# Kernel tuning notes

Hardware: AMD Instinct MI355X
Metric: run time of the kernel (lower is better)

## Reference

```python
import jax, jax.numpy as jnp
import numpy as np

TEMPERATURE = 11.313708498984761  # sqrt(128)


def setup_inputs() -> dict:
    key = jax.random.key(0)
    kq, kk, kv = jax.random.split(key, 3)
    b, n, m, d, dv = 16, 2048, 2048, 128, 128
    return {
        "queries": jax.random.normal(kq, (b, n, d), dtype=jnp.float32),
        "keys": jax.random.normal(kk, (b, m, d), dtype=jnp.float32),
        "values": jax.random.normal(kv, (b, m, dv), dtype=jnp.float32),
    }


def reference(queries, keys, values):
    # scores: [b, n, m]
    scores = jnp.einsum('bnd,bmd->bnm', queries, keys) / TEMPERATURE
    attn = jax.nn.softmax(scores, axis=2)
    # out: [b, n, d']
    return jnp.einsum('bnm,bmd->bnd', attn, values)
```

## Files before the change

kernel.cpp:

```cpp
#include <hip/hip_runtime.h>
#include <hip/hip_bf16.h>


#define BATCH 16
#define SEQ   2048
#define DIM   128

typedef short bf16x8 __attribute__((ext_vector_type(8)));
typedef float f32x16 __attribute__((ext_vector_type(16)));

static __device__ inline unsigned pk2(float lo, float hi) {
  union { float f; unsigned u; } a, b;
  a.f = lo; b.f = hi;
  return ((b.u + 0x8000u) & 0xffff0000u) | ((a.u + 0x8000u) >> 16);
}
static __device__ inline unsigned short f2bf(float f) {
  union { float f; unsigned u; } v; v.f = f;
  return (unsigned short)((v.u + 0x8000u) >> 16);
}
static __device__ inline float fast_exp2(float x) {
#if __has_builtin(__builtin_amdgcn_exp2f)
  return __builtin_amdgcn_exp2f(x);
#else
  return exp2f(x);
#endif
}

__global__ __launch_bounds__(256)
void prep_kernel(const float* __restrict__ K, const float* __restrict__ V,
                 unsigned short* __restrict__ Kb, unsigned short* __restrict__ Vt,
                 float scale) {
  const int bx = blockIdx.x, tid = threadIdx.x;
  if (bx < 2048) {
    size_t idx = (size_t)bx * 256 + tid;
    const float4* kf = (const float4*)K;
    float4 a = kf[idx * 2], c = kf[idx * 2 + 1];
    uint4 o;
    o.x = pk2(a.x * scale, a.y * scale);
    o.y = pk2(a.z * scale, a.w * scale);
    o.z = pk2(c.x * scale, c.y * scale);
    o.w = pk2(c.z * scale, c.w * scale);
    ((uint4*)Kb)[idx] = o;
  } else {
    __shared__ float tile[128][33];
    const int vb = bx - 2048;
    const int b = vb >> 6, r = vb & 63;
    const int m0 = (r & 15) * 128, d0 = (r >> 4) * 32;
    const int c = tid & 7, mr = tid >> 3;
    const float* src = V + ((size_t)(b * SEQ) + m0) * DIM + d0;
#pragma unroll
    for (int it = 0; it < 4; ++it) {
      int m = it * 32 + mr;
      float4 x = *(const float4*)(src + (size_t)m * DIM + c * 4);
      tile[m][c * 4 + 0] = x.x; tile[m][c * 4 + 1] = x.y;
      tile[m][c * 4 + 2] = x.z; tile[m][c * 4 + 3] = x.w;
    }
    __syncthreads();
    const int dr = tid >> 3, s = tid & 7;
    unsigned short* dst = Vt + ((size_t)(b * DIM) + d0 + dr) * SEQ + m0;
#pragma unroll
    for (int it = 0; it < 2; ++it) {
      int slot = it * 8 + s;
      uint4 o;
      o.x = pk2(tile[slot * 8 + 0][dr], tile[slot * 8 + 1][dr]);
      o.y = pk2(tile[slot * 8 + 2][dr], tile[slot * 8 + 3][dr]);
      o.z = pk2(tile[slot * 8 + 4][dr], tile[slot * 8 + 5][dr]);
      o.w = pk2(tile[slot * 8 + 6][dr], tile[slot * 8 + 7][dr]);
      *(uint4*)(dst + slot * 8) = o;
    }
  }
}

#define KS_OFF 0
#define VS_OFF 8704
#define PS_OFF 17920

__global__ __launch_bounds__(256, 2)
void attn_kernel(const float* __restrict__ Qf,
                 const unsigned short* __restrict__ Kb,
                 const unsigned short* __restrict__ Vtb,
                 float* __restrict__ out) {
  __shared__ __align__(16) unsigned short smem[22528];

  const int tid  = threadIdx.x;
  const int wv   = tid >> 6;
  const int w_q  = wv & 1;
  const int w_m  = wv >> 1;
  const int lane = tid & 63;
  const int l31  = lane & 31;
  const int q2   = lane >> 5;
  const int b    = blockIdx.x;
  const int q0   = blockIdx.y * 64 + w_q * 32;

  bf16x8 aq[8];
  {
    const float* qp = Qf + ((size_t)(b * SEQ) + q0 + l31) * DIM + q2 * 8;
#pragma unroll
    for (int c = 0; c < 8; ++c) {
      float4 x = *(const float4*)(qp + c * 16);
      float4 y = *(const float4*)(qp + c * 16 + 4);
      union { unsigned i[4]; bf16x8 v; } u;
      u.i[0] = pk2(x.x, x.y); u.i[1] = pk2(x.z, x.w);
      u.i[2] = pk2(y.x, y.y); u.i[3] = pk2(y.z, y.w);
      aq[c] = u.v;
    }
  }

  f32x16 oacc[4];
#pragma unroll
  for (int t = 0; t < 4; ++t)
#pragma unroll
    for (int i = 0; i < 16; ++i) oacc[t][i] = 0.0f;
  float lsum[16];
#pragma unroll
  for (int i = 0; i < 16; ++i) lsum[i] = 0.0f;

  const unsigned short* kb = Kb  + (size_t)b * SEQ * DIM;
  const unsigned short* vb = Vtb + (size_t)b * SEQ * DIM;
  unsigned short* ps = smem + PS_OFF + w_q * 2304;

  for (int kt = 0; kt < SEQ / 64; ++kt) {
    const int m0 = kt * 64;
    __syncthreads();
#pragma unroll
    for (int i = 0; i < 4; ++i) {
      int id = i * 256 + tid, row = id >> 4, c = id & 15;
      uint4 v = *(const uint4*)(kb + (size_t)(m0 + row) * DIM + c * 8);
      *(uint4*)(smem + KS_OFF + row * 136 + c * 8) = v;
    }
#pragma unroll
    for (int i = 0; i < 4; ++i) {
      int id = i * 256 + tid, dv = id >> 3, c = id & 7;
      uint4 v = *(const uint4*)(vb + (size_t)dv * SEQ + m0 + c * 8);
      *(uint4*)(smem + VS_OFF + dv * 72 + c * 8) = v;
    }
    __syncthreads();

    f32x16 s;
#pragma unroll
    for (int i = 0; i < 16; ++i) s[i] = 0.0f;
#pragma unroll
    for (int c = 0; c < 8; ++c) {
      bf16x8 bk = *(const bf16x8*)(smem + KS_OFF + (w_m * 32 + l31) * 136 + c * 16 + q2 * 8);
      s = __builtin_amdgcn_mfma_f32_32x32x16_bf16(aq[c], bk, s, 0, 0, 0);
    }

    float p[16];
#pragma unroll
    for (int i = 0; i < 16; ++i) { p[i] = fast_exp2(s[i]); lsum[i] += p[i]; }

#pragma unroll
    for (int r = 0; r < 16; ++r) {
      int qr = (r & 3) + ((r >> 2) << 3) + (q2 << 2);
      ps[qr * 72 + w_m * 32 + l31] = f2bf(p[r]);
    }
    asm volatile("s_waitcnt lgkmcnt(0)\n" ::: "memory");
    bf16x8 pf0 = *(const bf16x8*)(ps + l31 * 72 + w_m * 32 + q2 * 8);
    bf16x8 pf1 = *(const bf16x8*)(ps + l31 * 72 + w_m * 32 + 16 + q2 * 8);

#pragma unroll
    for (int t = 0; t < 4; ++t) {
      bf16x8 bv0 = *(const bf16x8*)(smem + VS_OFF + (t * 32 + l31) * 72 + w_m * 32 + q2 * 8);
      oacc[t] = __builtin_amdgcn_mfma_f32_32x32x16_bf16(pf0, bv0, oacc[t], 0, 0, 0);
      bf16x8 bv1 = *(const bf16x8*)(smem + VS_OFF + (t * 32 + l31) * 72 + w_m * 32 + 16 + q2 * 8);
      oacc[t] = __builtin_amdgcn_mfma_f32_32x32x16_bf16(pf1, bv1, oacc[t], 0, 0, 0);
    }
  }

#pragma unroll
  for (int r = 0; r < 16; ++r) {
    float v = lsum[r];
#pragma unroll
    for (int m = 1; m < 32; m <<= 1) v += __shfl_xor(v, m, 64);
    lsum[r] = v;
  }

  __syncthreads();
  float* cb  = (float*)smem;
  float* cbL = cb + 8192;
  if (w_m == 1) {
    float* my = cb + w_q * 4096;
#pragma unroll
    for (int t = 0; t < 4; ++t)
#pragma unroll
      for (int r = 0; r < 16; ++r)
        my[(t * 16 + r) * 64 + lane] = oacc[t][r];
    if (l31 == 0) {
#pragma unroll
      for (int r = 0; r < 16; ++r) {
        int qr = (r & 3) + ((r >> 2) << 3) + (q2 << 2);
        cbL[w_q * 32 + qr] = lsum[r];
      }
    }
  }
  __syncthreads();
  if (w_m == 0) {
    const float* pr = cb + w_q * 4096;
    float linv[16];
#pragma unroll
    for (int r = 0; r < 16; ++r) {
      int qr = (r & 3) + ((r >> 2) << 3) + (q2 << 2);
      linv[r] = 1.0f / (lsum[r] + cbL[w_q * 32 + qr]);
    }
    float* ob = out + ((size_t)(b * SEQ) + q0) * DIM;
#pragma unroll
    for (int t = 0; t < 4; ++t)
#pragma unroll
      for (int r = 0; r < 16; ++r) {
        int qr = (r & 3) + ((r >> 2) << 3) + (q2 << 2);
        ob[(size_t)qr * DIM + t * 32 + l31] = (oacc[t][r] + pr[(t * 16 + r) * 64 + lane]) * linv[r];
      }
  }
}

extern "C" void kernel_launch(void* const* d_in, const int* in_sizes, int n_in,
                              void* d_out, int out_size, void* d_ws, size_t ws_size,
                              hipStream_t stream) {
  const float* Q = (const float*)d_in[0];
  const float* K = (const float*)d_in[1];
  const float* V = (const float*)d_in[2];
  float* out = (float*)d_out;

  const size_t elems = (size_t)BATCH * SEQ * DIM;
  unsigned short* Kb = (unsigned short*)d_ws;
  unsigned short* Vt = Kb + elems;

  const double TEMPERATURE = 11.313708498984761;
  const float scale = (float)(1.4426950408889634 / TEMPERATURE);

  prep_kernel<<<3072, 256, 0, stream>>>(K, V, Kb, Vt, scale);
  attn_kernel<<<dim3(BATCH, SEQ / 64), 256, 0, stream>>>(Q, Kb, Vt, out);
}
```

Before: 142.1 us.

## Double-buffer K/V tiles via direct global-to-LDS loads and register P transpose

Replaces the synchronous register-staged K/V tile copies with global_load_lds direct-to-LDS loads into a double buffer, prefetching the next tile while computing the current one. LDS layouts use XOR swizzles instead of padding, to avoid bank conflicts. The score MFMA operands are swapped so P can be packed and redistributed with v_permlane32_swap instead of a round trip through LDS, which also reduces the row-sum bookkeeping to one scalar. Adds s_setprio around MFMA blocks; LDS use grows to 64KB per block, which may constrain occupancy.

```diff
diff --git a/kernel.cpp b/kernel.cpp
--- a/kernel.cpp
+++ b/kernel.cpp
@@ -1,29 +1,31 @@
 #include <hip/hip_runtime.h>
-#include <hip/hip_bf16.h>
 
 
 #define BATCH 16
 #define SEQ   2048
 #define DIM   128
+#define NT    (SEQ / 64)
 
 typedef short bf16x8 __attribute__((ext_vector_type(8)));
 typedef float f32x16 __attribute__((ext_vector_type(16)));
 
-static __device__ inline unsigned pk2(float lo, float hi) {
+static __device__ __forceinline__ unsigned pk2(float lo, float hi) {
   union { float f; unsigned u; } a, b;
   a.f = lo; b.f = hi;
   return ((b.u + 0x8000u) & 0xffff0000u) | ((a.u + 0x8000u) >> 16);
 }
-static __device__ inline unsigned short f2bf(float f) {
-  union { float f; unsigned u; } v; v.f = f;
-  return (unsigned short)((v.u + 0x8000u) >> 16);
-}
-static __device__ inline float fast_exp2(float x) {
+static __device__ __forceinline__ float fast_exp2(float x) {
 #if __has_builtin(__builtin_amdgcn_exp2f)
   return __builtin_amdgcn_exp2f(x);
 #else
   return exp2f(x);
 #endif
+}
+
+typedef __attribute__((address_space(1))) const unsigned int g_u32;
+typedef __attribute__((address_space(3))) unsigned int l_u32;
+static __device__ __forceinline__ void gl2lds16(const unsigned short* g, unsigned short* l) {
+  __builtin_amdgcn_global_load_lds((g_u32*)g, (l_u32*)l, 16, 0, 0);
 }
 
 __global__ __launch_bounds__(256)
@@ -71,16 +73,14 @@
   }
 }
 
-#define KS_OFF 0
-#define VS_OFF 8704
-#define PS_OFF 17920
 
 __global__ __launch_bounds__(256, 2)
 void attn_kernel(const float* __restrict__ Qf,
                  const unsigned short* __restrict__ Kb,
                  const unsigned short* __restrict__ Vtb,
                  float* __restrict__ out) {
-  __shared__ __align__(16) unsigned short smem[22528];
+  __shared__ __align__(1024) unsigned char smem[65536];
+  unsigned short* sm16 = (unsigned short*)smem;
 
   const int tid  = threadIdx.x;
   const int wv   = tid >> 6;
@@ -92,6 +92,9 @@
   const int b    = blockIdx.x;
   const int q0   = blockIdx.y * 64 + w_q * 32;
 
+  const unsigned short* kb = Kb  + (size_t)b * SEQ * DIM;
+  const unsigned short* vb = Vtb + (size_t)b * SEQ * DIM;
+
   bf16x8 aq[8];
   {
     const float* qp = Qf + ((size_t)(b * SEQ) + q0 + l31) * DIM + q2 * 8;
@@ -106,78 +109,91 @@
     }
   }
 
+  unsigned kgo[4], vgo[4];
+#pragma unroll
+  for (int i = 0; i < 4; ++i) {
+    int ch = wv * 4 + i;
+    int krow = ch * 4 + (lane >> 4);
+    kgo[i] = (unsigned)(krow * 128) + ((((lane & 15) << 4) ^ ((krow & 15) << 4)) >> 1);
+    int vrow = ch * 8 + (lane >> 3);
+    vgo[i] = (unsigned)(vrow * 2048) + ((((lane & 7) << 4) ^ ((vrow & 7) << 4)) >> 1);
+  }
+
+  const int kro = ((w_m * 32 + l31) << 8) + ((q2 << 4) ^ ((l31 & 15) << 4));
+  const int vro = (l31 << 7) + (((w_m << 6) + (q2 << 4)) ^ ((l31 & 7) << 4));
+
   f32x16 oacc[4];
 #pragma unroll
   for (int t = 0; t < 4; ++t)
 #pragma unroll
     for (int i = 0; i < 16; ++i) oacc[t][i] = 0.0f;
-  float lsum[16];
-#pragma unroll
-  for (int i = 0; i < 16; ++i) lsum[i] = 0.0f;
-
-  const unsigned short* kb = Kb  + (size_t)b * SEQ * DIM;
-  const unsigned short* vb = Vtb + (size_t)b * SEQ * DIM;
-  unsigned short* ps = smem + PS_OFF + w_q * 2304;
-
-  for (int kt = 0; kt < SEQ / 64; ++kt) {
-    const int m0 = kt * 64;
+  float lsum = 0.0f;
+
+#define STAGE(TK, BUF) do {                                                  \
+    const unsigned short* kt_b = kb + ((size_t)(TK) << 13);                  \
+    const unsigned short* vt_b = vb + ((TK) << 6);                           \
+    unsigned short* kd = sm16 + (((BUF) + wv * 4096) >> 1);                  \
+    unsigned short* vd = sm16 + ((32768 + (BUF) + wv * 4096) >> 1);          \
+    _Pragma("unroll")                                                        \
+    for (int i = 0; i < 4; ++i) gl2lds16(kt_b + kgo[i], kd + i * 512);       \
+    _Pragma("unroll")                                                        \
+    for (int i = 0; i < 4; ++i) gl2lds16(vt_b + vgo[i], vd + i * 512);       \
+  } while (0)
+
+  STAGE(0, 0);
+
+  for (int kt = 0; kt < NT; ++kt) {
+    const int cur = (kt & 1) << 14;
     __syncthreads();
-#pragma unroll
-    for (int i = 0; i < 4; ++i) {
-      int id = i * 256 + tid, row = id >> 4, c = id & 15;
-      uint4 v = *(const uint4*)(kb + (size_t)(m0 + row) * DIM + c * 8);
-      *(uint4*)(smem + KS_OFF + row * 136 + c * 8) = v;
-    }
-#pragma unroll
-    for (int i = 0; i < 4; ++i) {
-      int id = i * 256 + tid, dv = id >> 3, c = id & 7;
-      uint4 v = *(const uint4*)(vb + (size_t)dv * SEQ + m0 + c * 8);
-      *(uint4*)(smem + VS_OFF + dv * 72 + c * 8) = v;
-    }
-    __syncthreads();
+    if (kt + 1 < NT) STAGE(kt + 1, 16384 - cur);
+
+    const unsigned char* kB = smem + cur;
+    const unsigned char* vB = smem + 32768 + cur;
 
     f32x16 s;
 #pragma unroll
     for (int i = 0; i < 16; ++i) s[i] = 0.0f;
+    __builtin_amdgcn_s_setprio(1);
 #pragma unroll
     for (int c = 0; c < 8; ++c) {
-      bf16x8 bk = *(const bf16x8*)(smem + KS_OFF + (w_m * 32 + l31) * 136 + c * 16 + q2 * 8);
-      s = __builtin_amdgcn_mfma_f32_32x32x16_bf16(aq[c], bk, s, 0, 0, 0);
-    }
+      bf16x8 bk = *(const bf16x8*)(kB + (kro ^ (c << 5)));
+      s = __builtin_amdgcn_mfma_f32_32x32x16_bf16(bk, aq[c], s, 0, 0, 0);
+    }
+    __builtin_amdgcn_s_setprio(0);
 
     float p[16];
 #pragma unroll
-    for (int i = 0; i < 16; ++i) { p[i] = fast_exp2(s[i]); lsum[i] += p[i]; }
-
-#pragma unroll
-    for (int r = 0; r < 16; ++r) {
-      int qr = (r & 3) + ((r >> 2) << 3) + (q2 << 2);
-      ps[qr * 72 + w_m * 32 + l31] = f2bf(p[r]);
-    }
-    asm volatile("s_waitcnt lgkmcnt(0)\n" ::: "memory");
-    bf16x8 pf0 = *(const bf16x8*)(ps + l31 * 72 + w_m * 32 + q2 * 8);
-    bf16x8 pf1 = *(const bf16x8*)(ps + l31 * 72 + w_m * 32 + 16 + q2 * 8);
-
+    for (int i = 0; i < 16; ++i) { p[i] = fast_exp2(s[i]); lsum += p[i]; }
+
+    unsigned d0 = pk2(p[0], p[1]),   d1 = pk2(p[2], p[3]);
+    unsigned d2 = pk2(p[4], p[5]),   d3 = pk2(p[6], p[7]);
+    unsigned d4 = pk2(p[8], p[9]),   d5 = pk2(p[10], p[11]);
+    unsigned d6 = pk2(p[12], p[13]), d7 = pk2(p[14], p[15]);
+    asm("v_permlane32_swap_b32 %0, %1" : "+v"(d0), "+v"(d2));
+    asm("v_permlane32_swap_b32 %0, %1" : "+v"(d1), "+v"(d3));
+    asm("v_permlane32_swap_b32 %0, %1" : "+v"(d4), "+v"(d6));
+    asm("v_permlane32_swap_b32 %0, %1" : "+v"(d5), "+v"(d7));
+    union { unsigned u[4]; bf16x8 v; } pu0, pu1;
+    pu0.u[0] = d0; pu0.u[1] = d1; pu0.u[2] = d2; pu0.u[3] = d3;
+    pu1.u[0] = d4; pu1.u[1] = d5; pu1.u[2] = d6; pu1.u[3] = d7;
+
+    __builtin_amdgcn_s_setprio(1);
 #pragma unroll
     for (int t = 0; t < 4; ++t) {
-      bf16x8 bv0 = *(const bf16x8*)(smem + VS_OFF + (t * 32 + l31) * 72 + w_m * 32 + q2 * 8);
-      oacc[t] = __builtin_amdgcn_mfma_f32_32x32x16_bf16(pf0, bv0, oacc[t], 0, 0, 0);
-      bf16x8 bv1 = *(const bf16x8*)(smem + VS_OFF + (t * 32 + l31) * 72 + w_m * 32 + 16 + q2 * 8);
-      oacc[t] = __builtin_amdgcn_mfma_f32_32x32x16_bf16(pf1, bv1, oacc[t], 0, 0, 0);
-    }
-  }
-
-#pragma unroll
-  for (int r = 0; r < 16; ++r) {
-    float v = lsum[r];
-#pragma unroll
-    for (int m = 1; m < 32; m <<= 1) v += __shfl_xor(v, m, 64);
-    lsum[r] = v;
-  }
+      bf16x8 bv0 = *(const bf16x8*)(vB + t * 4096 + vro);
+      oacc[t] = __builtin_amdgcn_mfma_f32_32x32x16_bf16(pu0.v, bv0, oacc[t], 0, 0, 0);
+      bf16x8 bv1 = *(const bf16x8*)(vB + t * 4096 + (vro ^ 32));
+      oacc[t] = __builtin_amdgcn_mfma_f32_32x32x16_bf16(pu1.v, bv1, oacc[t], 0, 0, 0);
+    }
+    __builtin_amdgcn_s_setprio(0);
+  }
+#undef STAGE
+
+  lsum += __shfl_xor(lsum, 32, 64);
 
   __syncthreads();
   float* cb  = (float*)smem;
-  float* cbL = cb + 8192;
+  float* cbL = (float*)(smem + 32768);
   if (w_m == 1) {
     float* my = cb + w_q * 4096;
 #pragma unroll
@@ -185,14 +201,8 @@
 #pragma unroll
       for (int r = 0; r < 16; ++r)
         my[(t * 16 + r) * 64 + lane] = oacc[t][r];
-    if (l31 == 0) {
-#pragma unroll
-      for (int r = 0; r < 16; ++r) {
-        int qr = (r & 3) + ((r >> 2) << 3) + (q2 << 2);
-        cbL[w_q * 32 + qr] = lsum[r];
-      }
-    }
-  }
+  }
+  cbL[w_m * 64 + w_q * 32 + l31] = lsum;
   __syncthreads();
   if (w_m == 0) {
     const float* pr = cb + w_q * 4096;
@@ -200,7 +210,7 @@
 #pragma unroll
     for (int r = 0; r < 16; ++r) {
       int qr = (r & 3) + ((r >> 2) << 3) + (q2 << 2);
-      linv[r] = 1.0f / (lsum[r] + cbL[w_q * 32 + qr]);
+      linv[r] = 1.0f / (cbL[w_q * 32 + qr] + cbL[64 + w_q * 32 + qr]);
     }
     float* ob = out + ((size_t)(b * SEQ) + q0) * DIM;
 #pragma unroll
```

After: 136.5 us. 4.0% less time.
